# Kernel optimization log

Measured on AMD Instinct MI355X. Metric: run time of the kernel, lower is better.

The kernel has to match this reference:

```python
import jax, jax.numpy as jnp
import numpy as np

N_DIMS = 4          # len(dims): gauge-link channels split off by unpack_x
N_BANDS = 3         # SU(3) matrices
THRESHOLD = 1e-3    # trnorm_threshold
LAYER_CH = [6, 12, 12]  # input_channels + args.layer_channels


def cplx_einsum(eq, a, b):
    # complex einsum on real/imag-stacked tensors (last dim = 2)
    ar, ai = a[..., 0], a[..., 1]
    br, bi = b[..., 0], b[..., 1]
    re = jnp.einsum(eq, ar, br) - jnp.einsum(eq, ai, bi)
    im = jnp.einsum(eq, ar, bi) + jnp.einsum(eq, ai, br)
    return jnp.stack((re, im), axis=-1)


def h_conj(w):
    # hermitian conjugate: transpose matrix dims, negate imag part
    wt = jnp.swapaxes(w, -3, -2)
    return jnp.stack((wt[..., 0], -wt[..., 1]), axis=-1)


def gebl(x, weight):
    # x: [b, X, n_dims + n_in, nb, nb, 2]; weight: [n_out, w_in, w_in, 2]
    u, w = x[:, :, :N_DIMS], x[:, :, N_DIMS:]
    w = jnp.concatenate((w, h_conj(w)), axis=2)            # conjugation enlargement
    b, s = w.shape[0], w.shape[1]
    eye = jnp.zeros((N_BANDS, N_BANDS, 2), w.dtype).at[..., 0].set(jnp.eye(N_BANDS, dtype=w.dtype))
    unit = jnp.broadcast_to(eye, (b, s, 1, N_BANDS, N_BANDS, 2))
    w = jnp.concatenate((w, unit), axis=2)                 # unit elements
    ww = cplx_einsum('bxvij,bxwjk->bxvwik', w, w)          # pairwise matrix products
    w_out = cplx_einsum('uvw,bxvwij->bxuij', weight, ww)   # channel mixing
    return jnp.concatenate((u, w_out), axis=2)


def gerelu(x):
    u, w = x[:, :, :N_DIMS], x[:, :, N_DIMS:]
    tr_re = jnp.einsum('bxwiic->bxwc', w)[..., 0]          # Re(Tr W)
    w = jax.nn.relu(tr_re)[..., None, None, None] * w
    return jnp.concatenate((u, w), axis=2)


def trnorm(x):
    # trnorm_on_abs = True branch
    u, w = x[:, :, :N_DIMS], x[:, :, N_DIMS:]
    tr = jnp.einsum('bxviic->bxvc', w)
    tr_abs = jnp.sqrt(tr[..., 0] ** 2 + tr[..., 1] ** 2)
    norm = jnp.maximum(jnp.mean(tr_abs, axis=2), THRESHOLD)
    w = w / norm[:, :, None, None, None, None]
    return jnp.concatenate((u, w), axis=2)


def setup_inputs() -> dict:
    key = jax.random.key(0)
    ks = jax.random.split(key, 5)
    b, X = 2, 8 * 8 * 8 * 8
    x = jax.random.normal(ks[0], (b, X, N_DIMS + LAYER_CH[0], N_BANDS, N_BANDS, 2), jnp.float32)
    # GEBL weights: [n_out, w_in, w_in, 2], w_in = 2*n_in + 1
    w_in1 = 2 * LAYER_CH[0] + 1  # 13
    w_in2 = 2 * LAYER_CH[1] + 1  # 25
    w1 = jax.random.normal(ks[1], (LAYER_CH[1], w_in1, w_in1, 2), jnp.float32) * 0.1
    w2 = jax.random.normal(ks[2], (LAYER_CH[2], w_in2, w_in2, 2), jnp.float32) * 0.1
    dense_w = jax.random.normal(ks[3], (1, LAYER_CH[2] * 2), jnp.float32) * 0.2
    dense_b = jax.random.normal(ks[4], (1,), jnp.float32) * 0.01
    return {"x": x, "w1": w1, "w2": w2, "dense_w": dense_w, "dense_b": dense_b}


def reference(x, w1, w2, dense_w, dense_b):
    # GEBL -> GEReLU -> TrNorm (trnorm_before_ReLU=False), twice
    h = trnorm(gerelu(gebl(x, w1)))
    h = trnorm(gerelu(gebl(h, w2)))
    # Trace (normalized) -> reshape -> dense -> reshape
    w = h[:, :, N_DIMS:]
    tr = (1.0 / N_BANDS) * jnp.einsum('bxwiic->bxwc', w)   # [b, X, c, 2]
    flat = tr.reshape(-1, tr.shape[2] * 2)                 # torch .view: (c,2) interleaved
    out = flat @ dense_w.T + dense_b                        # [b*X, 1]
    return out.reshape(x.shape[0], -1)                      # [b, num_sites]
```

## Files before the change

kernel.cpp:

```cpp
#include <hip/hip_runtime.h>
#include <math.h>


#define NPTS 8192
#define THRESH 0.001f

typedef float f32x2 __attribute__((ext_vector_type(2)));

static __device__ __forceinline__ void cmacA(f32x2& acc, f32x2 cc, f32x2 ee) {
    asm("v_pk_fma_f32 %0, %1, %2, %0 op_sel:[0,0,0] op_sel_hi:[0,1,1]"
        : "+v"(acc) : "v"(cc), "v"(ee));
}
static __device__ __forceinline__ void cmacB(f32x2& acc, f32x2 cc, f32x2 ee) {
    asm("v_pk_fma_f32 %0, %1, %2, %0 op_sel:[1,1,0] op_sel_hi:[1,0,1] neg_lo:[1,0,0]"
        : "+v"(acc) : "v"(cc), "v"(ee));
}
static __device__ __forceinline__ void cmaccA(f32x2& acc, f32x2 A, f32x2 B) {
    asm("v_pk_fma_f32 %0, %1, %2, %0 op_sel:[0,0,0] op_sel_hi:[0,1,1] neg_hi:[1,0,0]"
        : "+v"(acc) : "v"(A), "v"(B));
}
static __device__ __forceinline__ void cmaccB(f32x2& acc, f32x2 A, f32x2 B) {
    asm("v_pk_fma_f32 %0, %1, %2, %0 op_sel:[1,1,0] op_sel_hi:[1,0,1]"
        : "+v"(acc) : "v"(A), "v"(B));
}
static __device__ __forceinline__ void cdotA(f32x2& acc, f32x2 gv, f32x2 cA) {
    asm("v_pk_fma_f32 %0, %1, %2, %0 op_sel:[0,0,0] op_sel_hi:[0,1,1]"
        : "+v"(acc) : "v"(gv), "v"(cA));
}
static __device__ __forceinline__ void cdotB(f32x2& acc, f32x2 gv, f32x2 cB) {
    asm("v_pk_fma_f32 %0, %1, %2, %0 op_sel:[1,0,0] op_sel_hi:[1,1,1]"
        : "+v"(acc) : "v"(gv), "v"(cB));
}

static __device__ __forceinline__ f32x2 c2(float2 a) {
    f32x2 r; r.x = a.x; r.y = a.y; return r;
}

__global__ void geblnet_setup(const float* __restrict__ w2,
                              float4* __restrict__ CTt) {
    int j = blockIdx.x * blockDim.x + threadIdx.x;
    if (j >= 12 * 169) return;
    int u = j / 169, it = j % 169;
    const float* W = w2 + u * 25 * 25 * 2;
#define WR(v, w) W[((v) * 25 + (w)) * 2]
#define WI(v, w) W[((v) * 25 + (w)) * 2 + 1]
    float c0, c1, c2v, c3;
    if (it < 78) {
        int q = it, a = 0;
        while (q >= 12 - a) { q -= 12 - a; ++a; }
        int b = a + q;
        float ar = WR(a, b) + (a != b ? WR(b, a) : 0.f);
        float ai = WI(a, b) + (a != b ? WI(b, a) : 0.f);
        float br = WR(12 + a, 12 + b) + (a != b ? WR(12 + b, 12 + a) : 0.f);
        float bi = WI(12 + a, 12 + b) + (a != b ? WI(12 + b, 12 + a) : 0.f);
        c0 = ar + br; c1 = bi - ai; c2v = ai + bi; c3 = ar - br;
    } else if (it < 156) {
        int q = it - 78, a = 0;
        while (q >= 12 - a) { q -= 12 - a; ++a; }
        int b = a + q;
        if (a != b) {
            float gr = WR(a, 12 + b) + WR(12 + b, a);
            float gi = WI(a, 12 + b) + WI(12 + b, a);
            float dr = WR(b, 12 + a) + WR(12 + a, b);
            float di = WI(b, 12 + a) + WI(12 + a, b);
            c0 = gr + dr; c1 = di - gi; c2v = gi + di; c3 = gr - dr;
        } else {
            float er = WR(a, 12 + a) + WR(12 + a, a);
            float ei = WI(a, 12 + a) + WI(12 + a, a);
            c0 = er; c1 = 0.f; c2v = ei; c3 = 0.f;
        }
    } else if (it < 168) {
        int a = it - 156;
        float fr = WR(a, 24) + WR(24, a), fi = WI(a, 24) + WI(24, a);
        float pr = WR(12 + a, 24) + WR(24, 12 + a);
        float pi = WI(12 + a, 24) + WI(24, 12 + a);
        c0 = fr + pr; c1 = pi - fi; c2v = fi + pi; c3 = fr - pr;
    } else {
        c0 = 3.f * WR(24, 24); c1 = 0.f; c2v = 3.f * WI(24, 24); c3 = 0.f;
    }
    CTt[it * 12 + u] = make_float4(c0, c2v, c1, c3);
#undef WR
#undef WI
}

union Scr {
    float2 bs[702];
    struct {
        float2 tpar[60];
        float2 tr1[12];
        float  sc1[12];
    } s;
};

__global__ __launch_bounds__(64) void geblnet_main(
    const float2* __restrict__ x2,
    const float2* __restrict__ w1g,
    const float* __restrict__ dw,
    const float* __restrict__ db,
    const float4* __restrict__ CTt,
    float* __restrict__ out)
{
    __shared__ float2 WeGV[170];
    __shared__ Scr S;
    __shared__ float2 Hs[108];

    const int t = threadIdx.x;
    const int p = blockIdx.x;

    if (t < 54) {
        int xc = t / 9, ik = t - xc * 9;
        int i = ik / 3, j = ik - i * 3;
        float2 val = x2[(size_t)p * 90 + 36 + t];
        WeGV[xc * 10 + ik] = val;
        WeGV[(6 + xc) * 10 + j * 3 + i] = make_float2(val.x, -val.y);
    } else if (t < 63) {
        int ik = t - 54;
        WeGV[120 + ik] = make_float2((ik % 4 == 0) ? 1.f : 0.f, 0.f);
    }
    __syncthreads();

    #pragma unroll 1
    for (int g = 0; g < 2; ++g) {
        const int u0 = g * 6;
        {
            int uu = 0, rem = t;
            #pragma unroll 2
            for (int e = t; e < 702; e += 64) {
                int v = rem / 9, jk = rem - v * 9;
                const float2* cp = w1g + ((u0 + uu) * 13 + v) * 13;
                f32x2 a0A = {0.f, 0.f}, a0B = {0.f, 0.f};
                f32x2 a1A = {0.f, 0.f}, a1B = {0.f, 0.f};
                #pragma unroll
                for (int w = 0; w < 12; w += 2) {
                    f32x2 c0 = c2(cp[w]),     e0 = c2(WeGV[w * 10 + jk]);
                    f32x2 c1 = c2(cp[w + 1]), e1 = c2(WeGV[(w + 1) * 10 + jk]);
                    cmacA(a0A, c0, e0);
                    cmacB(a0B, c0, e0);
                    cmacA(a1A, c1, e1);
                    cmacB(a1B, c1, e1);
                }
                {
                    f32x2 c0 = c2(cp[12]), e0 = c2(WeGV[120 + jk]);
                    cmacA(a0A, c0, e0);
                    cmacB(a0B, c0, e0);
                }
                S.bs[(uu * 13 + v) * 9 + jk] =
                    make_float2((a0A.x + a0B.x) + (a1A.x + a1B.x),
                                (a0A.y + a0B.y) + (a1A.y + a1B.y));
                rem += 64;
                if (rem >= 117) { rem -= 117; ++uu; }
            }
        }
        __syncthreads();
        if (t < 54) {
            int uu = t / 9, ik = t - uu * 9;
            int i = ik / 3, k = ik - i * 3;
            f32x2 h0A = {0.f, 0.f}, h0B = {0.f, 0.f};
            f32x2 h1A = {0.f, 0.f}, h1B = {0.f, 0.f};
            f32x2 h2A = {0.f, 0.f}, h2B = {0.f, 0.f};
            #pragma unroll
            for (int v = 0; v < 13; ++v) {
                const float2* a = &WeGV[v * 10 + i * 3];
                const float2* b = &S.bs[(uu * 13 + v) * 9 + k];
                f32x2 a0 = c2(a[0]), b0 = c2(b[0]);
                f32x2 a1 = c2(a[1]), b1 = c2(b[3]);
                f32x2 a2 = c2(a[2]), b2 = c2(b[6]);
                cmacA(h0A, a0, b0); cmacB(h0B, a0, b0);
                cmacA(h1A, a1, b1); cmacB(h1B, a1, b1);
                cmacA(h2A, a2, b2); cmacB(h2B, a2, b2);
            }
            Hs[(u0 + uu) * 9 + ik] =
                make_float2((h0A.x + h0B.x) + (h1A.x + h1B.x) + (h2A.x + h2B.x),
                            (h0A.y + h0B.y) + (h1A.y + h1B.y) + (h2A.y + h2B.y));
        }
        __syncthreads();
    }

    {
        float2 tt = make_float2(0.f, 0.f);
        float gg = 0.f, tra_v = 0.f;
        if (t < 12) {
            float2 a = Hs[t * 9 + 0], b = Hs[t * 9 + 4], c = Hs[t * 9 + 8];
            tt = make_float2(a.x + b.x + c.x, a.y + b.y + c.y);
            gg = tt.x > 0.f ? tt.x : 0.f;
            tra_v = gg * sqrtf(tt.x * tt.x + tt.y * tt.y);
        }
        float m = tra_v;
        m += __shfl_xor(m, 1, 16);
        m += __shfl_xor(m, 2, 16);
        m += __shfl_xor(m, 4, 16);
        m += __shfl_xor(m, 8, 16);
        if (t < 12) {
            S.s.tr1[t] = tt;
            S.s.sc1[t] = gg / fmaxf(m * (1.f / 12.f), THRESH);
        }
    }
    __syncthreads();

    for (int it = t; it < 169; it += 64) {
        float2 val;
        if (it < 156) {
            int q = it < 78 ? it : it - 78;
            float fs = sqrtf(625.0f - 8.0f * (float)q);
            int a = (int)((25.0f - fs) * 0.5f);
            int b = q - (a * (25 - a)) / 2 + a;
            const float2* Ha = &Hs[a * 9];
            const float2* Hb = &Hs[b * 9];
            float s = S.s.sc1[a] * S.s.sc1[b];
            f32x2 v0A = {0.f, 0.f}, v0B = {0.f, 0.f};
            f32x2 v1A = {0.f, 0.f}, v1B = {0.f, 0.f};
            if (it < 78) {
                #pragma unroll
                for (int i = 0; i < 3; ++i)
                    #pragma unroll
                    for (int jj = 0; jj < 3; ++jj) {
                        f32x2 A = c2(Ha[i * 3 + jj]), B = c2(Hb[jj * 3 + i]);
                        if (((i * 3 + jj) & 1) == 0) {
                            cmacA(v0A, A, B); cmacB(v0B, A, B);
                        } else {
                            cmacA(v1A, A, B); cmacB(v1B, A, B);
                        }
                    }
            } else {
                #pragma unroll
                for (int e = 0; e < 9; ++e) {
                    f32x2 A = c2(Ha[e]), B = c2(Hb[e]);
                    if ((e & 1) == 0) { cmaccA(v0A, A, B); cmaccB(v0B, A, B); }
                    else              { cmaccA(v1A, A, B); cmaccB(v1B, A, B); }
                }
            }
            val = make_float2(s * ((v0A.x + v0B.x) + (v1A.x + v1B.x)),
                              s * ((v0A.y + v0B.y) + (v1A.y + v1B.y)));
        } else if (it < 168) {
            int a = it - 156;
            float s = S.s.sc1[a]; float2 tt = S.s.tr1[a];
            val = make_float2(s * tt.x, s * tt.y);
        } else {
            val = make_float2(1.f, 0.f);
        }
        WeGV[it] = val;
    }
    __syncthreads();

    if (t < 60) {
        int q = t / 12, u = t - q * 12;
        int i0 = q * 34, i1 = (q == 4) ? 169 : i0 + 34;
        f32x2 A0 = {0.f, 0.f}, B0 = {0.f, 0.f};
        f32x2 A1 = {0.f, 0.f}, B1 = {0.f, 0.f};
        f32x2 A2 = {0.f, 0.f}, B2 = {0.f, 0.f};
        f32x2 A3 = {0.f, 0.f}, B3 = {0.f, 0.f};
        int it = i0;
        #pragma unroll 1
        for (; it + 4 <= i1; it += 4) {
            float4 c0v = CTt[(it + 0) * 12 + u];
            float4 c1v = CTt[(it + 1) * 12 + u];
            float4 c2c = CTt[(it + 2) * 12 + u];
            float4 c3v = CTt[(it + 3) * 12 + u];
            f32x2 g0 = c2(WeGV[it + 0]), g1 = c2(WeGV[it + 1]);
            f32x2 g2 = c2(WeGV[it + 2]), g3 = c2(WeGV[it + 3]);
            f32x2 cA, cB;
            cA.x = c0v.x; cA.y = c0v.y; cB.x = c0v.z; cB.y = c0v.w;
            cdotA(A0, g0, cA); cdotB(B0, g0, cB);
            cA.x = c1v.x; cA.y = c1v.y; cB.x = c1v.z; cB.y = c1v.w;
            cdotA(A1, g1, cA); cdotB(B1, g1, cB);
            cA.x = c2c.x; cA.y = c2c.y; cB.x = c2c.z; cB.y = c2c.w;
            cdotA(A2, g2, cA); cdotB(B2, g2, cB);
            cA.x = c3v.x; cA.y = c3v.y; cB.x = c3v.z; cB.y = c3v.w;
            cdotA(A3, g3, cA); cdotB(B3, g3, cB);
        }
        for (; it < i1; ++it) {
            float4 c = CTt[it * 12 + u];
            f32x2 cA, cB;
            cA.x = c.x; cA.y = c.y; cB.x = c.z; cB.y = c.w;
            f32x2 g = c2(WeGV[it]);
            cdotA(A0, g, cA); cdotB(B0, g, cB);
        }
        S.s.tpar[u * 5 + q] =
            make_float2(((A0.x + B0.x) + (A1.x + B1.x)) +
                        ((A2.x + B2.x) + (A3.x + B3.x)),
                        ((A0.y + B0.y) + (A1.y + B1.y)) +
                        ((A2.y + B2.y) + (A3.y + B3.y)));
    }
    __syncthreads();

    {
        float2 tt = make_float2(0.f, 0.f);
        float gg = 0.f, tra_v = 0.f;
        if (t < 12) {
            #pragma unroll
            for (int q = 0; q < 5; ++q) {
                float2 A = S.s.tpar[t * 5 + q];
                tt.x += A.x; tt.y += A.y;
            }
            gg = tt.x > 0.f ? tt.x : 0.f;
            tra_v = gg * sqrtf(tt.x * tt.x + tt.y * tt.y);
        }
        float m = tra_v;
        m += __shfl_xor(m, 1, 16);
        m += __shfl_xor(m, 2, 16);
        m += __shfl_xor(m, 4, 16);
        m += __shfl_xor(m, 8, 16);
        float term = 0.f;
        if (t < 12) {
            float inv = 1.f / fmaxf(m * (1.f / 12.f), THRESH);
            float s = gg * inv * (1.f / 3.f);
            term = s * (tt.x * dw[2 * t] + tt.y * dw[2 * t + 1]);
        }
        term += __shfl_xor(term, 1, 16);
        term += __shfl_xor(term, 2, 16);
        term += __shfl_xor(term, 4, 16);
        term += __shfl_xor(term, 8, 16);
        if (t == 0) out[p] = term + db[0];
    }
}

extern "C" void kernel_launch(void* const* d_in, const int* in_sizes, int n_in,
                              void* d_out, int out_size, void* d_ws, size_t ws_size,
                              hipStream_t stream) {
    const float* x  = (const float*)d_in[0];
    const float* w1 = (const float*)d_in[1];
    const float* w2 = (const float*)d_in[2];
    const float* dw = (const float*)d_in[3];
    const float* db = (const float*)d_in[4];
    float* outp = (float*)d_out;
    float4* CTt = (float4*)d_ws;

    geblnet_setup<<<(12 * 169 + 255) / 256, 256, 0, stream>>>(w2, CTt);

    geblnet_main<<<NPTS, 64, 0, stream>>>(
        (const float2*)x, (const float2*)w1, dw, db, CTt, outp);
}
```

Baseline: 117.4 us.

## Pack four sites per block, one wavefront each, replacing barriers with waitcnt

Each 256-thread block now processes four lattice sites, one per 64-lane wavefront, with per-wave shared-memory slices. Block-wide __syncthreads barriers become wave-local s_waitcnt lgkmcnt(0) waits, since each site's data is touched only by its own wave. This is meant to cut barrier and workgroup-dispatch overhead across the 8192 sites. Correctness depends on intra-wave lockstep execution and the compiler not reordering LDS accesses around the inline asm.

```diff
diff --git a/kernel.cpp b/kernel.cpp
--- a/kernel.cpp
+++ b/kernel.cpp
@@ -6,6 +6,10 @@
 #define THRESH 0.001f
 
 typedef float f32x2 __attribute__((ext_vector_type(2)));
+
+static __device__ __forceinline__ void wsync() {
+    asm volatile("s_waitcnt lgkmcnt(0)" ::: "memory");
+}
 
 static __device__ __forceinline__ void cmacA(f32x2& acc, f32x2 cc, f32x2 ee) {
     asm("v_pk_fma_f32 %0, %1, %2, %0 op_sel:[0,0,0] op_sel_hi:[0,1,1]"
@@ -92,7 +96,7 @@
     } s;
 };
 
-__global__ __launch_bounds__(64) void geblnet_main(
+__global__ __launch_bounds__(256) void geblnet_main(
     const float2* __restrict__ x2,
     const float2* __restrict__ w1g,
     const float* __restrict__ dw,
@@ -100,12 +104,17 @@
     const float4* __restrict__ CTt,
     float* __restrict__ out)
 {
-    __shared__ float2 WeGV[170];
-    __shared__ Scr S;
-    __shared__ float2 Hs[108];
-
-    const int t = threadIdx.x;
-    const int p = blockIdx.x;
+    __shared__ float2 WeGV_[4][170];
+    __shared__ Scr S_[4];
+    __shared__ float2 Hs_[4][108];
+
+    const int wid = threadIdx.x >> 6;
+    const int t = threadIdx.x & 63;
+    const int p = blockIdx.x * 4 + wid;
+
+    float2* WeGV = WeGV_[wid];
+    Scr* Sp = &S_[wid];
+    float2* Hs = Hs_[wid];
 
     if (t < 54) {
         int xc = t / 9, ik = t - xc * 9;
@@ -117,7 +126,7 @@
         int ik = t - 54;
         WeGV[120 + ik] = make_float2((ik % 4 == 0) ? 1.f : 0.f, 0.f);
     }
-    __syncthreads();
+    wsync();
 
     #pragma unroll 1
     for (int g = 0; g < 2; ++g) {
@@ -144,14 +153,14 @@
                     cmacA(a0A, c0, e0);
                     cmacB(a0B, c0, e0);
                 }
-                S.bs[(uu * 13 + v) * 9 + jk] =
+                Sp->bs[(uu * 13 + v) * 9 + jk] =
                     make_float2((a0A.x + a0B.x) + (a1A.x + a1B.x),
                                 (a0A.y + a0B.y) + (a1A.y + a1B.y));
                 rem += 64;
                 if (rem >= 117) { rem -= 117; ++uu; }
             }
         }
-        __syncthreads();
+        wsync();
         if (t < 54) {
             int uu = t / 9, ik = t - uu * 9;
             int i = ik / 3, k = ik - i * 3;
@@ -161,7 +170,7 @@
             #pragma unroll
             for (int v = 0; v < 13; ++v) {
                 const float2* a = &WeGV[v * 10 + i * 3];
-                const float2* b = &S.bs[(uu * 13 + v) * 9 + k];
+                const float2* b = &Sp->bs[(uu * 13 + v) * 9 + k];
                 f32x2 a0 = c2(a[0]), b0 = c2(b[0]);
                 f32x2 a1 = c2(a[1]), b1 = c2(b[3]);
                 f32x2 a2 = c2(a[2]), b2 = c2(b[6]);
@@ -173,7 +182,7 @@
                 make_float2((h0A.x + h0B.x) + (h1A.x + h1B.x) + (h2A.x + h2B.x),
                             (h0A.y + h0B.y) + (h1A.y + h1B.y) + (h2A.y + h2B.y));
         }
-        __syncthreads();
+        wsync();
     }
 
     {
@@ -191,11 +200,11 @@
         m += __shfl_xor(m, 4, 16);
         m += __shfl_xor(m, 8, 16);
         if (t < 12) {
-            S.s.tr1[t] = tt;
-            S.s.sc1[t] = gg / fmaxf(m * (1.f / 12.f), THRESH);
-        }
-    }
-    __syncthreads();
+            Sp->s.tr1[t] = tt;
+            Sp->s.sc1[t] = gg / fmaxf(m * (1.f / 12.f), THRESH);
+        }
+    }
+    wsync();
 
     for (int it = t; it < 169; it += 64) {
         float2 val;
@@ -206,7 +215,7 @@
             int b = q - (a * (25 - a)) / 2 + a;
             const float2* Ha = &Hs[a * 9];
             const float2* Hb = &Hs[b * 9];
-            float s = S.s.sc1[a] * S.s.sc1[b];
+            float s = Sp->s.sc1[a] * Sp->s.sc1[b];
             f32x2 v0A = {0.f, 0.f}, v0B = {0.f, 0.f};
             f32x2 v1A = {0.f, 0.f}, v1B = {0.f, 0.f};
             if (it < 78) {
@@ -233,14 +242,14 @@
                               s * ((v0A.y + v0B.y) + (v1A.y + v1B.y)));
         } else if (it < 168) {
             int a = it - 156;
-            float s = S.s.sc1[a]; float2 tt = S.s.tr1[a];
+            float s = Sp->s.sc1[a]; float2 tt = Sp->s.tr1[a];
             val = make_float2(s * tt.x, s * tt.y);
         } else {
             val = make_float2(1.f, 0.f);
         }
         WeGV[it] = val;
     }
-    __syncthreads();
+    wsync();
 
     if (t < 60) {
         int q = t / 12, u = t - q * 12;
@@ -275,13 +284,13 @@
             f32x2 g = c2(WeGV[it]);
             cdotA(A0, g, cA); cdotB(B0, g, cB);
         }
-        S.s.tpar[u * 5 + q] =
+        Sp->s.tpar[u * 5 + q] =
             make_float2(((A0.x + B0.x) + (A1.x + B1.x)) +
                         ((A2.x + B2.x) + (A3.x + B3.x)),
                         ((A0.y + B0.y) + (A1.y + B1.y)) +
                         ((A2.y + B2.y) + (A3.y + B3.y)));
     }
-    __syncthreads();
+    wsync();
 
     {
         float2 tt = make_float2(0.f, 0.f);
@@ -289,7 +298,7 @@
         if (t < 12) {
             #pragma unroll
             for (int q = 0; q < 5; ++q) {
-                float2 A = S.s.tpar[t * 5 + q];
+                float2 A = Sp->s.tpar[t * 5 + q];
                 tt.x += A.x; tt.y += A.y;
             }
             gg = tt.x > 0.f ? tt.x : 0.f;
@@ -327,6 +336,6 @@
 
     geblnet_setup<<<(12 * 169 + 255) / 256, 256, 0, stream>>>(w2, CTt);
 
-    geblnet_main<<<NPTS, 64, 0, stream>>>(
+    geblnet_main<<<NPTS / 4, 256, 0, stream>>>(
         (const float2*)x, (const float2*)w1, dw, db, CTt, outp);
 }
```

Result: no change. 115.2 us (median of 2 runs) (-1.9%).
